# Optimization experiments

Measured on AMD Instinct MI355X. Metric: run time of the kernel, lower is better.

Reference implementation:

```python
import jax, jax.numpy as jnp
import numpy as np

B, N = 16, 128
DN0, DE0, DH = 64, 16, 128  # input node dim, input edge dim, hidden dim


def _gnn2(A, x, e, w_msg, b_msg, w_node, b_node):
    """One GNN2 layer on dense batched graphs.
    A: [B,N,N] adjacency mask, x: [B,N,Dn], e: [B,N,N,De].
    Message/new-edge: relu(Linear([x_i, x_j, e_ij])) masked by A.
    New node: relu(Linear([x, sum_j msg_ij])).
    The concat-Linear is decomposed into three matmuls to avoid
    materializing the [B,N,N,2Dn+De] concat tensor.
    """
    Dn = x.shape[-1]
    Wi, Wj, We = w_msg[:Dn], w_msg[Dn:2 * Dn], w_msg[2 * Dn:]
    xi = x @ Wi                                   # [B,N,Do]
    xj = x @ Wj                                   # [B,N,Do]
    msg = jax.nn.relu(xi[:, :, None, :] + xj[:, None, :, :] + e @ We + b_msg)
    msg = msg * A[..., None]                      # mask non-edges -> new edge_attr [B,N,N,Do]
    agg = msg.sum(axis=2)                         # scatter-sum over neighbors j -> [B,N,Do]
    Wx, Wa = w_node[:Dn], w_node[Dn:]
    x_new = jax.nn.relu(x @ Wx + agg @ Wa + b_node)
    return x_new, msg


def setup_inputs() -> dict:
    key = jax.random.key(0)
    ks = iter(jax.random.split(key, 32))
    s = 0.05
    inp = {
        "edge_index": jax.random.randint(next(ks), (B, N, N), 0, 2, dtype=jnp.int32),
        "x": jax.random.normal(next(ks), (B, N, DN0), dtype=jnp.float32),
        "edge_attr": jax.random.normal(next(ks), (B, N, N, DE0), dtype=jnp.float32),
    }
    def w(shape):
        return s * jax.random.normal(next(ks), shape, dtype=jnp.float32)
    # layer 0: node_in=64, edge_in=16 -> 128
    inp["w_msg_0"], inp["b_msg_0"] = w((2 * DN0 + DE0, DH)), w((DH,))
    inp["w_node_0"], inp["b_node_0"] = w((DN0 + DH, DH)), w((DH,))
    # layers 1,2: 128 -> 128
    for l in (1, 2):
        inp[f"w_msg_{l}"], inp[f"b_msg_{l}"] = w((2 * DH + DH, DH)), w((DH,))
        inp[f"w_node_{l}"], inp[f"b_node_{l}"] = w((DH + DH, DH)), w((DH,))
    # head mlp: 128 -> 128 -> 128 -> 1
    inp["w_h1"], inp["b_h1"] = w((DH, DH)), w((DH,))
    inp["w_h2"], inp["b_h2"] = w((DH, DH)), w((DH,))
    inp["w_h3"], inp["b_h3"] = w((DH, 1)), w((1,))
    return inp


def reference(edge_index, x, edge_attr,
              w_msg_0, b_msg_0, w_node_0, b_node_0,
              w_msg_1, b_msg_1, w_node_1, b_node_1,
              w_msg_2, b_msg_2, w_node_2, b_node_2,
              w_h1, b_h1, w_h2, b_h2, w_h3, b_h3):
    A = edge_index.astype(jnp.float32)
    x = x.astype(jnp.float32)
    # layer 0
    x, e = _gnn2(A, x, edge_attr, w_msg_0, b_msg_0, w_node_0, b_node_0)
    # middle layer with 0.5 residual blend
    x_, e_ = _gnn2(A, x, e, w_msg_1, b_msg_1, w_node_1, b_node_1)
    x = 0.5 * (x + x_)
    e = 0.5 * (e + e_)
    # last layer
    x, e = _gnn2(A, x, e, w_msg_2, b_msg_2, w_node_2, b_node_2)
    # edge_mean readout + MLP head
    h = e.mean(axis=(1, 2))                       # [B, DH]
    h = jax.nn.relu(h @ w_h1 + b_h1)
    h = jax.nn.relu(h @ w_h2 + b_h2)
    out = h @ w_h3 + b_h3                         # [B, 1]
    return out.squeeze(-1)                        # [B]
```

## Files before the change

### kernel.cpp

```cpp
#include <hip/hip_runtime.h>

constexpr int B = 16, N = 128, D = 128, DN0 = 64, DE0 = 16;

typedef _Float16 half8 __attribute__((ext_vector_type(8)));
typedef _Float16 half4 __attribute__((ext_vector_type(4)));
typedef float floatx4 __attribute__((ext_vector_type(4)));
typedef float floatx16 __attribute__((ext_vector_type(16)));

__device__ __forceinline__ void gld16(const _Float16* g, _Float16* l) {
  __builtin_amdgcn_global_load_lds(
      (const __attribute__((address_space(1))) void*)g,
      (__attribute__((address_space(3))) void*)l, 16, 0, 0);
}

__global__ __launch_bounds__(256) void k_pre(
    const float* __restrict__ x, const float* __restrict__ wm0,
    const float* __restrict__ bm0, const float* __restrict__ wm1,
    const float* __restrict__ wm2,
    float* __restrict__ xi0, float* __restrict__ xj0,
    _Float16* __restrict__ weT1, _Float16* __restrict__ weT2) {
  const int bid = blockIdx.x;
  const int t = threadIdx.x;
  if (bid < B * N) {
    const int row = bid;
    const int half = t >> 7, c = t & 127;
    __shared__ float xr[DN0];
    if (t < DN0) xr[t] = x[(size_t)row * DN0 + t];
    __syncthreads();
    float a = half ? 0.f : bm0[c];
    const float* wb = wm0 + half * DN0 * D;
    #pragma unroll 32
    for (int k = 0; k < DN0; ++k) a = fmaf(xr[k], wb[k * D + c], a);
    (half ? xj0 : xi0)[(size_t)row * D + c] = a;
  } else {
    const int g = (bid - B * N) * 256 + t;
    const int layer = g >> 14;
    const int rem = g & 16383;
    const int c = rem >> 7, k = rem & 127;
    const float* src = layer ? wm2 : wm1;
    _Float16* dst = layer ? weT2 : weT1;
    dst[rem] = (_Float16)src[(2 * D + k) * D + c];
  }
}

__global__ __launch_bounds__(256) void k_edge0(
    const int* __restrict__ ei, const float* __restrict__ eattr,
    const float* __restrict__ wm0, const float* __restrict__ x0,
    const float* __restrict__ xi0, const float* __restrict__ xj0,
    const float* __restrict__ wn0, const float* __restrict__ bn0,
    const float* __restrict__ wm1, const float* __restrict__ bm1,
    _Float16* __restrict__ msg0, float* __restrict__ x1,
    float* __restrict__ xi1, float* __restrict__ xj1) {
  const int row = blockIdx.x;
  const int b = row >> 7;
  const int t = threadIdx.x;
  const int c8 = (t & 15) * 8, jr = t >> 4;

  __shared__ float eb[N * 20];
  __shared__ float w_t[DE0][D];
  __shared__ float amask[N];
  __shared__ float xi_r[D];
  __shared__ float sX0[DN0], sAgg[D], sPart[2][D], sX1[D];
  float* hp = eb;

  const float4* esrc = (const float4*)(eattr + (size_t)row * N * DE0);
  const float4* wsrc = (const float4*)(wm0 + 2 * DN0 * D);
  #pragma unroll
  for (int u = 0; u < 2; ++u) {
    const int idx4 = u * 256 + t;
    const int j = idx4 >> 2;
    const int k4 = (idx4 & 3) * 4;
    *(float4*)&eb[j * 20 + k4] = esrc[idx4];
    ((float4*)&w_t[0][0])[idx4] = wsrc[idx4];
  }
  if (t < N) {
    amask[t] = (float)ei[(size_t)row * N + t];
    xi_r[t] = xi0[(size_t)row * D + t];
  } else if (t < N + DN0) {
    sX0[t - N] = x0[(size_t)row * DN0 + (t - N)];
  }
  __syncthreads();

  float acc[8][8] = {};
  #pragma unroll 4
  for (int k = 0; k < DE0; ++k) {
    float av[8];
    #pragma unroll
    for (int p = 0; p < 8; ++p) av[p] = eb[(16 * p + jr) * 20 + k];
    const floatx4 wv0 = *(const floatx4*)&w_t[k][c8];
    const floatx4 wv1 = *(const floatx4*)&w_t[k][c8 + 4];
    #pragma unroll
    for (int p = 0; p < 8; ++p)
      #pragma unroll
      for (int q = 0; q < 4; ++q) {
        acc[p][q]     = fmaf(av[p], wv0[q], acc[p][q]);
        acc[p][4 + q] = fmaf(av[p], wv1[q], acc[p][4 + q]);
      }
  }

  float acc8[8] = {};
  const float* xjb = xj0 + (size_t)b * N * D;
  _Float16* mrow = msg0 + (size_t)row * N * D;
  const floatx4 xiv0 = *(const floatx4*)&xi_r[c8];
  const floatx4 xiv1 = *(const floatx4*)&xi_r[c8 + 4];
  #pragma unroll
  for (int p = 0; p < 8; ++p) {
    const int j = 16 * p + jr;
    const float am = amask[j];
    const floatx4 xjv0 = *(const floatx4*)&xjb[j * D + c8];
    const floatx4 xjv1 = *(const floatx4*)&xjb[j * D + c8 + 4];
    half8 hv;
    #pragma unroll
    for (int q = 0; q < 4; ++q) {
      float v0 = fmaxf(xiv0[q] + xjv0[q] + acc[p][q], 0.f) * am;
      float v1 = fmaxf(xiv1[q] + xjv1[q] + acc[p][4 + q], 0.f) * am;
      hv[q] = (_Float16)v0;
      hv[4 + q] = (_Float16)v1;
      acc8[q] += v0;
      acc8[4 + q] += v1;
    }
    if (am != 0.f)
      *(half8*)&mrow[j * D + (((t & 15) ^ jr) << 3)] = hv;
  }

  __syncthreads();
  #pragma unroll
  for (int q = 0; q < 8; ++q) hp[(jr * 16 + (t & 15)) * 8 + q] = acc8[q];
  __syncthreads();
  if (t < D) {
    float s = 0.f;
    #pragma unroll
    for (int g = 0; g < 16; ++g) s += hp[(g * 16 + (t >> 3)) * 8 + (t & 7)];
    sAgg[t] = s;
  }
  __syncthreads();

  const int half = t >> 7, c = t & 127;
  {
    float a;
    if (half == 0) {
      a = bn0[c];
      #pragma unroll 32
      for (int k = 0; k < DN0; ++k) a = fmaf(sX0[k], wn0[k * D + c], a);
      #pragma unroll
      for (int k = 0; k < 32; ++k) a = fmaf(sAgg[k], wn0[(DN0 + k) * D + c], a);
    } else {
      a = 0.f;
      #pragma unroll 32
      for (int k = 32; k < D; ++k) a = fmaf(sAgg[k], wn0[(DN0 + k) * D + c], a);
    }
    sPart[half][c] = a;
  }
  __syncthreads();
  if (t < D) {
    const float v = fmaxf(sPart[0][t] + sPart[1][t], 0.f);
    x1[(size_t)row * D + t] = v;
    sX1[t] = v;
  }
  __syncthreads();

  {
    float aa = half ? 0.f : bm1[c];
    const float* wh = wm1 + half * D * D;
    #pragma unroll 32
    for (int k = 0; k < D; ++k) aa = fmaf(sX1[k], wh[k * D + c], aa);
    (half ? xj1 : xi1)[(size_t)row * D + c] = aa;
  }
}

__global__ __launch_bounds__(256, 2) void k_mid(
    const int* __restrict__ ei, const _Float16* __restrict__ weT1,
    const _Float16* __restrict__ weT2,
    const float* __restrict__ xi, const float* __restrict__ xj,
    const float* __restrict__ x1,
    const float* __restrict__ wn1, const float* __restrict__ bn1,
    const float* __restrict__ wm2, const float* __restrict__ bm2,
    _Float16* __restrict__ em,
    float* __restrict__ xi2, float* __restrict__ xj2) {
  const int row = blockIdx.x;
  const int b = row >> 7;
  const int t = threadIdx.x;
  const int w = t >> 6;
  const int lane = t & 63;
  const int l31 = lane & 31;
  const int l15 = lane & 15;
  const int hl = lane >> 5;

  __shared__ _Float16 sE[N * D];
  __shared__ float sMask[N];
  __shared__ float sAgg[D], sX1[D], sPart[2][D], sX2[D];

  const _Float16* gsrc = em + (size_t)row * N * D;
  #pragma unroll
  for (int u = 0; u < 8; ++u) {
    const int seg = (u * 4 + w) * 512;
    gld16(gsrc + seg + lane * 8, &sE[seg]);
  }

  half8 a1[8];
  #pragma unroll
  for (int ks = 0; ks < 8; ++ks)
    a1[ks] = *(const half8*)(weT1 + (32 * w + l31) * D + 16 * ks + 8 * hl);

  floatx4 xiv[4];
  #pragma unroll
  for (int g = 0; g < 4; ++g)
    xiv[g] = *(const floatx4*)&xi[(size_t)row * D + 32 * w + 8 * g + 4 * hl];
  if (t < N) sMask[t] = (float)ei[(size_t)row * N + t];
  else if (t < N + D) sX1[t - N] = x1[(size_t)row * D + (t - N)];

  __syncthreads();

  float am[4];
  #pragma unroll
  for (int jt = 0; jt < 4; ++jt) am[jt] = sMask[32 * jt + l31];

  const floatx16 vzero = {0.f,0.f,0.f,0.f,0.f,0.f,0.f,0.f,
                          0.f,0.f,0.f,0.f,0.f,0.f,0.f,0.f};
  floatx16 acc[4];
  #pragma unroll
  for (int jt = 0; jt < 4; ++jt) acc[jt] = vzero;
  #pragma unroll
  for (int ks = 0; ks < 8; ++ks)
    #pragma unroll
    for (int jt = 0; jt < 4; ++jt) {
      const half8 bv = *(const half8*)
          &sE[(32 * jt + l31) * D + (((2 * ks + hl) ^ l15) << 3)];
      acc[jt] = __builtin_amdgcn_mfma_f32_32x32x16_f16(a1[ks], bv, acc[jt], 0, 0, 0);
    }

  __syncthreads();

  const float* xjb = xj + (size_t)b * N * D;
  floatx4 hacc[4];
  #pragma unroll
  for (int g = 0; g < 4; ++g) hacc[g] = (floatx4){0.f, 0.f, 0.f, 0.f};
  #pragma unroll
  for (int jt = 0; jt < 4; ++jt) {
    const int j = 32 * jt + l31;
    #pragma unroll
    for (int g = 0; g < 4; ++g) {
      const int cofs = 32 * w + 8 * g + 4 * hl;
      const int hidx = j * D + (((4 * w + g) ^ l15) << 3) + 4 * hl;
      const floatx4 xjv = *(const floatx4*)&xjb[j * D + cofs];
      const half4 m0 = *(const half4*)&sE[hidx];
      half4 mid;
      floatx4 m1;
      #pragma unroll
      for (int r = 0; r < 4; ++r) {
        const float v = xiv[g][r] + xjv[r] + acc[jt][4 * g + r];
        m1[r] = fmaxf(v, 0.f) * am[jt];
        mid[r] = (_Float16)(0.5f * ((float)m0[r] + m1[r]));
      }
      *(half4*)&sE[hidx] = mid;
      hacc[g] += m1;
    }
  }

  #pragma unroll
  for (int m = 1; m < 32; m <<= 1)
    #pragma unroll
    for (int g = 0; g < 4; ++g)
      #pragma unroll
      for (int r = 0; r < 4; ++r)
        hacc[g][r] += __shfl_xor(hacc[g][r], m, 64);
  if (l31 == 0) {
    #pragma unroll
    for (int g = 0; g < 4; ++g)
      *(floatx4*)&sAgg[32 * w + 8 * g + 4 * hl] = hacc[g];
  }

  half8 a2[8];
  #pragma unroll
  for (int ks = 0; ks < 8; ++ks)
    a2[ks] = *(const half8*)(weT2 + (32 * w + l31) * D + 16 * ks + 8 * hl);

  __syncthreads();

  #pragma unroll
  for (int jt = 0; jt < 4; ++jt) acc[jt] = vzero;
  #pragma unroll
  for (int ks = 0; ks < 8; ++ks)
    #pragma unroll
    for (int jt = 0; jt < 4; ++jt) {
      const half8 bv = *(const half8*)
          &sE[(32 * jt + l31) * D + (((2 * ks + hl) ^ l15) << 3)];
      acc[jt] = __builtin_amdgcn_mfma_f32_32x32x16_f16(a2[ks], bv, acc[jt], 0, 0, 0);
    }

  __syncthreads();

  #pragma unroll
  for (int jt = 0; jt < 4; ++jt) {
    const int j = 32 * jt + l31;
    #pragma unroll
    for (int g = 0; g < 4; ++g) {
      const int hidx = j * D + (((4 * w + g) ^ l15) << 3) + 4 * hl;
      half4 tv;
      #pragma unroll
      for (int r = 0; r < 4; ++r) tv[r] = (_Float16)acc[jt][4 * g + r];
      *(half4*)&sE[hidx] = tv;
    }
  }

  __syncthreads();

  uint4* gdst = (uint4*)(em + (size_t)row * N * D);
  const uint4* ls = (const uint4*)sE;
  #pragma unroll
  for (int u = 0; u < 8; ++u) {
    const int idx4 = u * 256 + t;
    const int j = u * 16 + (t >> 4);
    if (sMask[j] != 0.f) gdst[idx4] = ls[idx4];
  }

  const int half = t >> 7, c = t & 127;
  {
    float a;
    if (half == 0) {
      a = bn1[c];
      #pragma unroll 32
      for (int k = 0; k < D; ++k) a = fmaf(sX1[k], wn1[k * D + c], a);
    } else {
      a = 0.f;
      #pragma unroll 32
      for (int k = 0; k < D; ++k) a = fmaf(sAgg[k], wn1[(D + k) * D + c], a);
    }
    sPart[half][c] = a;
  }
  __syncthreads();
  if (t < D)
    sX2[t] = 0.5f * (sX1[t] + fmaxf(sPart[0][t] + sPart[1][t], 0.f));
  __syncthreads();
  {
    float aa = half ? 0.f : bm2[c];
    const float* wh = wm2 + half * D * D;
    #pragma unroll 32
    for (int k = 0; k < D; ++k) aa = fmaf(sX2[k], wh[k * D + c], aa);
    (half ? xj2 : xi2)[(size_t)row * D + c] = aa;
  }
}

__global__ __launch_bounds__(256) void k_fin(
    const int* __restrict__ ei, const _Float16* __restrict__ t2,
    const float* __restrict__ xi, const float* __restrict__ xj,
    float* __restrict__ rowsum) {
  const int row = blockIdx.x;
  const int b = row >> 7;
  const int t = threadIdx.x;
  const int c8 = (t & 15) * 8, jr = t >> 4;

  __shared__ float sMask[N];
  __shared__ float hp[16][16][8];
  if (t < N) sMask[t] = (float)ei[(size_t)row * N + t];
  float xiv[8];
  *(floatx4*)&xiv[0] = *(const floatx4*)&xi[row * D + c8];
  *(floatx4*)&xiv[4] = *(const floatx4*)&xi[row * D + c8 + 4];
  __syncthreads();

  const _Float16* src = t2 + (size_t)row * N * D;
  const float* xjb = xj + (size_t)b * N * D;
  float acc8[8] = {};
  #pragma unroll
  for (int u = 0; u < 8; ++u) {
    const int j = u * 16 + jr;
    if (sMask[j] != 0.f) {
      const half8 tv = *(const half8*)(src + j * D + (((t & 15) ^ jr) << 3));
      const floatx4 xj0 = *(const floatx4*)&xjb[j * D + c8];
      const floatx4 xj1 = *(const floatx4*)&xjb[j * D + c8 + 4];
      #pragma unroll
      for (int r = 0; r < 4; ++r) {
        acc8[r]     += fmaxf(xiv[r] + xj0[r] + (float)tv[r], 0.f);
        acc8[4 + r] += fmaxf(xiv[4 + r] + xj1[r] + (float)tv[4 + r], 0.f);
      }
    }
  }
  #pragma unroll
  for (int k = 0; k < 8; ++k) hp[jr][t & 15][k] = acc8[k];
  __syncthreads();
  if (t < D) {
    float s = 0.f;
    #pragma unroll
    for (int g = 0; g < 16; ++g) s += hp[g][t >> 3][t & 7];
    rowsum[row * D + t] = s;
  }
}

__global__ __launch_bounds__(128) void k_head(
    const float* __restrict__ rowsum,
    const float* __restrict__ w1, const float* __restrict__ b1,
    const float* __restrict__ w2, const float* __restrict__ b2,
    const float* __restrict__ w3, const float* __restrict__ b3,
    float* __restrict__ out) {
  const int b = blockIdx.x;
  const int c = threadIdx.x;
  __shared__ float hr[D], h1r[D], h2r[D];
  const float* rs = rowsum + (size_t)b * N * D;
  float s = 0.f;
  for (int i = 0; i < N; ++i) s += rs[i * D + c];
  hr[c] = s * (1.f / (N * N));
  __syncthreads();
  float a = b1[c];
  #pragma unroll 8
  for (int k = 0; k < D; ++k) a = fmaf(hr[k], w1[k * D + c], a);
  h1r[c] = fmaxf(a, 0.f);
  __syncthreads();
  a = b2[c];
  #pragma unroll 8
  for (int k = 0; k < D; ++k) a = fmaf(h1r[k], w2[k * D + c], a);
  h2r[c] = fmaxf(a, 0.f);
  __syncthreads();
  hr[c] = h2r[c] * w3[c];
  __syncthreads();
  if (c == 0) {
    float s2 = b3[0];
    for (int k = 0; k < D; ++k) s2 += hr[k];
    out[b] = s2;
  }
}

extern "C" void kernel_launch(void* const* d_in, const int* in_sizes, int n_in,
                              void* d_out, int out_size, void* d_ws, size_t ws_size,
                              hipStream_t stream) {
  const int*   ei  = (const int*)d_in[0];
  const float* x0  = (const float*)d_in[1];
  const float* ea  = (const float*)d_in[2];
  const float* wm0 = (const float*)d_in[3];
  const float* bm0 = (const float*)d_in[4];
  const float* wn0 = (const float*)d_in[5];
  const float* bn0 = (const float*)d_in[6];
  const float* wm1 = (const float*)d_in[7];
  const float* bm1 = (const float*)d_in[8];
  const float* wn1 = (const float*)d_in[9];
  const float* bn1 = (const float*)d_in[10];
  const float* wm2 = (const float*)d_in[11];
  const float* bm2 = (const float*)d_in[12];
  const float* wh1 = (const float*)d_in[15];
  const float* bh1 = (const float*)d_in[16];
  const float* wh2 = (const float*)d_in[17];
  const float* bh2 = (const float*)d_in[18];
  const float* wh3 = (const float*)d_in[19];
  const float* bh3 = (const float*)d_in[20];
  float* out = (float*)d_out;

  _Float16* msg0h = (_Float16*)d_ws;
  _Float16* weT1  = msg0h + (size_t)B * N * N * D;
  _Float16* weT2  = weT1 + D * D;
  float* f = (float*)(weT2 + D * D);
  size_t off = 0;
  const size_t R = (size_t)B * N * D;
  float* xi0  = f + off; off += R;
  float* xj0  = f + off; off += R;
  float* x1   = f + off; off += R;
  float* xi1  = f + off; off += R;
  float* xj1  = f + off; off += R;
  float* xi2  = f + off; off += R;
  float* xj2  = f + off; off += R;
  float* rsum = f + off; off += R;

  const int rows = B * N;
  k_pre  <<<rows + 128, 256, 0, stream>>>(x0, wm0, bm0, wm1, wm2,
                                          xi0, xj0, weT1, weT2);
  k_edge0<<<rows, 256, 0, stream>>>(ei, ea, wm0, x0, xi0, xj0,
                                    wn0, bn0, wm1, bm1,
                                    msg0h, x1, xi1, xj1);
  k_mid  <<<rows, 256, 0, stream>>>(ei, weT1, weT2, xi1, xj1, x1,
                                    wn1, bn1, wm2, bm2,
                                    msg0h, xi2, xj2);
  k_fin  <<<rows, 256, 0, stream>>>(ei, msg0h, xi2, xj2, rsum);
  k_head <<<B,    128, 0, stream>>>(rsum, wh1, bh1, wh2, bh2, wh3, bh3, out);
}
```

Baseline: 221.0 us.

## Split per-row node updates into separate batched kernels with weight reuse

The node-update and next-layer projection matvecs move out of the edge kernels into new kernels, k_node1 and k_node2. Each new kernel processes 8 rows per block, so every weight load is reused across several rows instead of being reloaded for each row. The edge kernels now only write the aggregated messages to global memory, which shortens their tails and frees LDS and registers. The cost is two extra kernel launches and a round trip of the aggregates through global memory, with the rsum buffer reused as scratch.

```diff
diff --git a/kernel.cpp b/kernel.cpp
--- a/kernel.cpp
+++ b/kernel.cpp
@@ -45,12 +45,9 @@
 
 __global__ __launch_bounds__(256) void k_edge0(
     const int* __restrict__ ei, const float* __restrict__ eattr,
-    const float* __restrict__ wm0, const float* __restrict__ x0,
+    const float* __restrict__ wm0,
     const float* __restrict__ xi0, const float* __restrict__ xj0,
-    const float* __restrict__ wn0, const float* __restrict__ bn0,
-    const float* __restrict__ wm1, const float* __restrict__ bm1,
-    _Float16* __restrict__ msg0, float* __restrict__ x1,
-    float* __restrict__ xi1, float* __restrict__ xj1) {
+    _Float16* __restrict__ msg0, float* __restrict__ agg0) {
   const int row = blockIdx.x;
   const int b = row >> 7;
   const int t = threadIdx.x;
@@ -60,7 +57,6 @@
   __shared__ float w_t[DE0][D];
   __shared__ float amask[N];
   __shared__ float xi_r[D];
-  __shared__ float sX0[DN0], sAgg[D], sPart[2][D], sX1[D];
   float* hp = eb;
 
   const float4* esrc = (const float4*)(eattr + (size_t)row * N * DE0);
@@ -76,8 +72,6 @@
   if (t < N) {
     amask[t] = (float)ei[(size_t)row * N + t];
     xi_r[t] = xi0[(size_t)row * D + t];
-  } else if (t < N + DN0) {
-    sX0[t - N] = x0[(size_t)row * DN0 + (t - N)];
   }
   __syncthreads();
 
@@ -131,52 +125,90 @@
     float s = 0.f;
     #pragma unroll
     for (int g = 0; g < 16; ++g) s += hp[(g * 16 + (t >> 3)) * 8 + (t & 7)];
-    sAgg[t] = s;
-  }
-  __syncthreads();
-
-  const int half = t >> 7, c = t & 127;
-  {
-    float a;
-    if (half == 0) {
-      a = bn0[c];
-      #pragma unroll 32
-      for (int k = 0; k < DN0; ++k) a = fmaf(sX0[k], wn0[k * D + c], a);
-      #pragma unroll
-      for (int k = 0; k < 32; ++k) a = fmaf(sAgg[k], wn0[(DN0 + k) * D + c], a);
-    } else {
-      a = 0.f;
-      #pragma unroll 32
-      for (int k = 32; k < D; ++k) a = fmaf(sAgg[k], wn0[(DN0 + k) * D + c], a);
-    }
-    sPart[half][c] = a;
-  }
-  __syncthreads();
-  if (t < D) {
-    const float v = fmaxf(sPart[0][t] + sPart[1][t], 0.f);
-    x1[(size_t)row * D + t] = v;
-    sX1[t] = v;
-  }
-  __syncthreads();
-
-  {
-    float aa = half ? 0.f : bm1[c];
-    const float* wh = wm1 + half * D * D;
-    #pragma unroll 32
-    for (int k = 0; k < D; ++k) aa = fmaf(sX1[k], wh[k * D + c], aa);
-    (half ? xj1 : xi1)[(size_t)row * D + c] = aa;
-  }
+    agg0[(size_t)row * D + t] = s;
+  }
+}
+
+__global__ __launch_bounds__(256) void k_node1(
+    const float* __restrict__ x0, const float* __restrict__ agg0,
+    const float* __restrict__ wn0, const float* __restrict__ bn0,
+    const float* __restrict__ wm1, const float* __restrict__ bm1,
+    float* __restrict__ x1, float* __restrict__ xi1, float* __restrict__ xj1) {
+  const int r0 = blockIdx.x * 8;
+  const int t = threadIdx.x;
+  const int c = t & 127, rh = t >> 7;
+  __shared__ float sIn[8][DN0];
+  __shared__ float sAg[8][D];
+  __shared__ float sX1[8][D];
+  ((float2*)&sIn[0][0])[t] = ((const float2*)(x0 + (size_t)r0 * DN0))[t];
+  ((float4*)&sAg[0][0])[t] = ((const float4*)(agg0 + (size_t)r0 * D))[t];
+  __syncthreads();
+
+  float acc[4];
+  #pragma unroll
+  for (int r = 0; r < 4; ++r) acc[r] = bn0[c];
+  #pragma unroll 4
+  for (int k4 = 0; k4 < DN0; k4 += 4) {
+    const float* wb = wn0 + k4 * D + c;
+    const float w0 = wb[0], w1 = wb[D], w2 = wb[2 * D], w3 = wb[3 * D];
+    #pragma unroll
+    for (int r = 0; r < 4; ++r) {
+      const float4 xv = *(const float4*)&sIn[rh * 4 + r][k4];
+      acc[r] = fmaf(xv.x, w0, acc[r]);
+      acc[r] = fmaf(xv.y, w1, acc[r]);
+      acc[r] = fmaf(xv.z, w2, acc[r]);
+      acc[r] = fmaf(xv.w, w3, acc[r]);
+    }
+  }
+  #pragma unroll 4
+  for (int k4 = 0; k4 < D; k4 += 4) {
+    const float* wb = wn0 + (DN0 + k4) * D + c;
+    const float w0 = wb[0], w1 = wb[D], w2 = wb[2 * D], w3 = wb[3 * D];
+    #pragma unroll
+    for (int r = 0; r < 4; ++r) {
+      const float4 xv = *(const float4*)&sAg[rh * 4 + r][k4];
+      acc[r] = fmaf(xv.x, w0, acc[r]);
+      acc[r] = fmaf(xv.y, w1, acc[r]);
+      acc[r] = fmaf(xv.z, w2, acc[r]);
+      acc[r] = fmaf(xv.w, w3, acc[r]);
+    }
+  }
+  #pragma unroll
+  for (int r = 0; r < 4; ++r) {
+    const float v = fmaxf(acc[r], 0.f);
+    sX1[rh * 4 + r][c] = v;
+    x1[(size_t)(r0 + rh * 4 + r) * D + c] = v;
+  }
+  __syncthreads();
+
+  float a[8];
+  #pragma unroll
+  for (int r = 0; r < 8; ++r) a[r] = rh ? 0.f : bm1[c];
+  const float* wh = wm1 + (size_t)rh * D * D;
+  #pragma unroll 2
+  for (int k4 = 0; k4 < D; k4 += 4) {
+    const float* wb = wh + k4 * D + c;
+    const float w0 = wb[0], w1 = wb[D], w2 = wb[2 * D], w3 = wb[3 * D];
+    #pragma unroll
+    for (int r = 0; r < 8; ++r) {
+      const float4 xv = *(const float4*)&sX1[r][k4];
+      a[r] = fmaf(xv.x, w0, a[r]);
+      a[r] = fmaf(xv.y, w1, a[r]);
+      a[r] = fmaf(xv.z, w2, a[r]);
+      a[r] = fmaf(xv.w, w3, a[r]);
+    }
+  }
+  float* dst = rh ? xj1 : xi1;
+  #pragma unroll
+  for (int r = 0; r < 8; ++r) dst[(size_t)(r0 + r) * D + c] = a[r];
 }
 
 __global__ __launch_bounds__(256, 2) void k_mid(
     const int* __restrict__ ei, const _Float16* __restrict__ weT1,
     const _Float16* __restrict__ weT2,
     const float* __restrict__ xi, const float* __restrict__ xj,
-    const float* __restrict__ x1,
-    const float* __restrict__ wn1, const float* __restrict__ bn1,
-    const float* __restrict__ wm2, const float* __restrict__ bm2,
     _Float16* __restrict__ em,
-    float* __restrict__ xi2, float* __restrict__ xj2) {
+    float* __restrict__ agg1) {
   const int row = blockIdx.x;
   const int b = row >> 7;
   const int t = threadIdx.x;
@@ -188,7 +220,6 @@
 
   __shared__ _Float16 sE[N * D];
   __shared__ float sMask[N];
-  __shared__ float sAgg[D], sX1[D], sPart[2][D], sX2[D];
 
   const _Float16* gsrc = em + (size_t)row * N * D;
   #pragma unroll
@@ -207,7 +238,6 @@
   for (int g = 0; g < 4; ++g)
     xiv[g] = *(const floatx4*)&xi[(size_t)row * D + 32 * w + 8 * g + 4 * hl];
   if (t < N) sMask[t] = (float)ei[(size_t)row * N + t];
-  else if (t < N + D) sX1[t - N] = x1[(size_t)row * D + (t - N)];
 
   __syncthreads();
 
@@ -267,7 +297,7 @@
   if (l31 == 0) {
     #pragma unroll
     for (int g = 0; g < 4; ++g)
-      *(floatx4*)&sAgg[32 * w + 8 * g + 4 * hl] = hacc[g];
+      *(floatx4*)&agg1[(size_t)row * D + 32 * w + 8 * g + 4 * hl] = hacc[g];
   }
 
   half8 a2[8];
@@ -313,32 +343,79 @@
     const int j = u * 16 + (t >> 4);
     if (sMask[j] != 0.f) gdst[idx4] = ls[idx4];
   }
-
-  const int half = t >> 7, c = t & 127;
-  {
-    float a;
-    if (half == 0) {
-      a = bn1[c];
-      #pragma unroll 32
-      for (int k = 0; k < D; ++k) a = fmaf(sX1[k], wn1[k * D + c], a);
-    } else {
-      a = 0.f;
-      #pragma unroll 32
-      for (int k = 0; k < D; ++k) a = fmaf(sAgg[k], wn1[(D + k) * D + c], a);
-    }
-    sPart[half][c] = a;
-  }
-  __syncthreads();
-  if (t < D)
-    sX2[t] = 0.5f * (sX1[t] + fmaxf(sPart[0][t] + sPart[1][t], 0.f));
-  __syncthreads();
-  {
-    float aa = half ? 0.f : bm2[c];
-    const float* wh = wm2 + half * D * D;
-    #pragma unroll 32
-    for (int k = 0; k < D; ++k) aa = fmaf(sX2[k], wh[k * D + c], aa);
-    (half ? xj2 : xi2)[(size_t)row * D + c] = aa;
-  }
+}
+
+__global__ __launch_bounds__(256) void k_node2(
+    const float* __restrict__ x1, const float* __restrict__ agg1,
+    const float* __restrict__ wn1, const float* __restrict__ bn1,
+    const float* __restrict__ wm2, const float* __restrict__ bm2,
+    float* __restrict__ xi2, float* __restrict__ xj2) {
+  const int r0 = blockIdx.x * 8;
+  const int t = threadIdx.x;
+  const int c = t & 127, rh = t >> 7;
+  __shared__ float sIn[8][D];
+  __shared__ float sAg[8][D];
+  __shared__ float sXm[8][D];
+  ((float4*)&sIn[0][0])[t] = ((const float4*)(x1 + (size_t)r0 * D))[t];
+  ((float4*)&sAg[0][0])[t] = ((const float4*)(agg1 + (size_t)r0 * D))[t];
+  __syncthreads();
+
+  float acc[4];
+  #pragma unroll
+  for (int r = 0; r < 4; ++r) acc[r] = bn1[c];
+  #pragma unroll 4
+  for (int k4 = 0; k4 < D; k4 += 4) {
+    const float* wb = wn1 + k4 * D + c;
+    const float w0 = wb[0], w1 = wb[D], w2 = wb[2 * D], w3 = wb[3 * D];
+    #pragma unroll
+    for (int r = 0; r < 4; ++r) {
+      const float4 xv = *(const float4*)&sIn[rh * 4 + r][k4];
+      acc[r] = fmaf(xv.x, w0, acc[r]);
+      acc[r] = fmaf(xv.y, w1, acc[r]);
+      acc[r] = fmaf(xv.z, w2, acc[r]);
+      acc[r] = fmaf(xv.w, w3, acc[r]);
+    }
+  }
+  #pragma unroll 4
+  for (int k4 = 0; k4 < D; k4 += 4) {
+    const float* wb = wn1 + (D + k4) * D + c;
+    const float w0 = wb[0], w1 = wb[D], w2 = wb[2 * D], w3 = wb[3 * D];
+    #pragma unroll
+    for (int r = 0; r < 4; ++r) {
+      const float4 xv = *(const float4*)&sAg[rh * 4 + r][k4];
+      acc[r] = fmaf(xv.x, w0, acc[r]);
+      acc[r] = fmaf(xv.y, w1, acc[r]);
+      acc[r] = fmaf(xv.z, w2, acc[r]);
+      acc[r] = fmaf(xv.w, w3, acc[r]);
+    }
+  }
+  #pragma unroll
+  for (int r = 0; r < 4; ++r) {
+    const float v = 0.5f * (sIn[rh * 4 + r][c] + fmaxf(acc[r], 0.f));
+    sXm[rh * 4 + r][c] = v;
+  }
+  __syncthreads();
+
+  float a[8];
+  #pragma unroll
+  for (int r = 0; r < 8; ++r) a[r] = rh ? 0.f : bm2[c];
+  const float* wh = wm2 + (size_t)rh * D * D;
+  #pragma unroll 2
+  for (int k4 = 0; k4 < D; k4 += 4) {
+    const float* wb = wh + k4 * D + c;
+    const float w0 = wb[0], w1 = wb[D], w2 = wb[2 * D], w3 = wb[3 * D];
+    #pragma unroll
+    for (int r = 0; r < 8; ++r) {
+      const float4 xv = *(const float4*)&sXm[r][k4];
+      a[r] = fmaf(xv.x, w0, a[r]);
+      a[r] = fmaf(xv.y, w1, a[r]);
+      a[r] = fmaf(xv.z, w2, a[r]);
+      a[r] = fmaf(xv.w, w3, a[r]);
+    }
+  }
+  float* dst = rh ? xj2 : xi2;
+  #pragma unroll
+  for (int r = 0; r < 8; ++r) dst[(size_t)(r0 + r) * D + c] = a[r];
 }
 
 __global__ __launch_bounds__(256) void k_fin(
@@ -458,15 +535,17 @@
   float* xj2  = f + off; off += R;
   float* rsum = f + off; off += R;
 
+  float* aggS = rsum;
+
   const int rows = B * N;
   k_pre  <<<rows + 128, 256, 0, stream>>>(x0, wm0, bm0, wm1, wm2,
                                           xi0, xj0, weT1, weT2);
-  k_edge0<<<rows, 256, 0, stream>>>(ei, ea, wm0, x0, xi0, xj0,
-                                    wn0, bn0, wm1, bm1,
-                                    msg0h, x1, xi1, xj1);
-  k_mid  <<<rows, 256, 0, stream>>>(ei, weT1, weT2, xi1, xj1, x1,
-                                    wn1, bn1, wm2, bm2,
-                                    msg0h, xi2, xj2);
+  k_edge0<<<rows, 256, 0, stream>>>(ei, ea, wm0, xi0, xj0, msg0h, aggS);
+  k_node1<<<rows / 8, 256, 0, stream>>>(x0, aggS, wn0, bn0, wm1, bm1,
+                                        x1, xi1, xj1);
+  k_mid  <<<rows, 256, 0, stream>>>(ei, weT1, weT2, xi1, xj1, msg0h, aggS);
+  k_node2<<<rows / 8, 256, 0, stream>>>(x1, aggS, wn1, bn1, wm2, bm2,
+                                        xi2, xj2);
   k_fin  <<<rows, 256, 0, stream>>>(ei, msg0h, xi2, xj2, rsum);
   k_head <<<B,    128, 0, stream>>>(rsum, wh1, bh1, wh2, bh2, wh3, bh3, out);
 }
```

Result: no change. 222.4 us (+0.6%).
